# Kernel optimization log

Measured on AMD Instinct MI355X. Metric: run time of the kernel, lower is better.

Reference implementation:

```python
import jax, jax.numpy as jnp
import numpy as np

DIM = 1536
NH = 12
HD = 128
EPS = 1e-6


def _rope(x, freqs, f, h, w, start):
    # x: [B,S,N,D] with S == f*h*w; freqs: [1024, D//2, 2] (real, imag) unit rotations
    B, S, N, D = x.shape
    c = D // 2
    c0 = c - 2 * (c // 3)
    c1 = c // 3
    ff = jnp.broadcast_to(freqs[start:start + f, :c0][:, None, None], (f, h, w, c0, 2))
    fh = jnp.broadcast_to(freqs[:h, c0:c0 + c1][None, :, None], (f, h, w, c1, 2))
    fw = jnp.broadcast_to(freqs[:w, c0 + c1:c][None, None, :], (f, h, w, c1, 2))
    fr = jnp.concatenate([ff, fh, fw], axis=3).reshape(S, 1, c, 2)  # [S,1,c,2]
    xr, xi = x[..., 0::2], x[..., 1::2]          # interleaved real/imag pairs
    cr, ci = fr[None, ..., 0], fr[None, ..., 1]  # [1,S,1,c]
    yr = xr * cr - xi * ci
    yi = xr * ci + xi * cr
    return jnp.stack([yr, yi], axis=-1).reshape(B, S, N, D)


def _rms(x, g):
    return x * jax.lax.rsqrt(jnp.mean(x * x, axis=-1, keepdims=True) + EPS) * g


def setup_inputs():
    key = jax.random.key(0)
    ks = jax.random.split(key, 16)
    S = 3 * 30 * 52  # chunk_size = 3 frames * 1560 tokens/frame
    x = jax.random.normal(ks[0], (1, S, DIM), jnp.float32)
    fr = jax.random.normal(ks[1], (1024, HD // 2, 2), jnp.float32)
    fr = fr / jnp.sqrt(jnp.sum(fr * fr, axis=-1, keepdims=True) + 1e-12)  # unit-modulus rotations
    g_kmean = jax.random.uniform(ks[2], (1, NH, HD), jnp.float32)  # mean of relu(k): nonnegative
    g_kv = jax.random.normal(ks[3], (1, NH, HD, HD), jnp.float32) * 0.05
    p = lambda i, shp: jax.random.normal(ks[i], shp, jnp.float32) * 0.02
    return dict(
        x=x, freqs=fr, g_kmean=g_kmean, g_kv=g_kv,
        Wq=p(4, (DIM, DIM)), bq=p(5, (DIM,)),
        Wk=p(6, (DIM, DIM)), bk=p(7, (DIM,)),
        Wv=p(8, (DIM, DIM)), bv=p(9, (DIM,)),
        Wo=p(10, (DIM, DIM)), bo=p(11, (DIM,)),
        gq=jnp.ones((DIM,), jnp.float32), gk=jnp.ones((DIM,), jnp.float32),
        Wlin=p(12, (HD, HD)), blin=p(13, (HD,)),
        f_frames=3, h_grid=30, w_grid=52,
    )


def reference(x, freqs, g_kmean, g_kv, Wq, bq, Wk, bk, Wv, bv, Wo, bo, gq, gk, Wlin, blin, f_frames, h_grid, w_grid):
    B, S, _ = x.shape
    q = _rms(x @ Wq.T + bq, gq).reshape(B, S, NH, HD)
    k = _rms(x @ Wk.T + bk, gk).reshape(B, S, NH, HD)
    v = (x @ Wv.T + bv).reshape(B, S, NH, HD)
    rq = _rope(q, freqs, f_frames, h_grid, w_grid, 0)
    rk = _rope(k, freqs, f_frames, h_grid, w_grid, 0)
    # local window attention: at step 0 (current_start=0, empty cache, sink_size=0)
    # the working kv window is exactly the roped current chunk
    scores = jnp.einsum('bsnd,btnd->bnst', rq, rk) * (HD ** -0.5)
    x_local = jnp.einsum('bnst,btnd->bsnd', jax.nn.softmax(scores, axis=-1), v)
    # global linear-attention branch (kernel_func = relu feature map on q, roped q against kv state)
    qf = jax.nn.relu(q)
    z = 1.0 / (jnp.einsum('bsnd,bnd->bsn', qf, g_kmean) + 1e-6)
    xg = jnp.einsum('bsnd,bndm->bsnm', rq, g_kv) * z[..., None]
    xg = xg @ Wlin.T + blin
    out = (x_local + xg).reshape(B, S, DIM) @ Wo.T + bo
    return out
```

## Files before the change

### kernel.cpp

```cpp
#include <hip/hip_runtime.h>

typedef short s16x8 __attribute__((ext_vector_type(8)));
typedef float f32x4 __attribute__((ext_vector_type(4)));
typedef unsigned short u16x4 __attribute__((ext_vector_type(4)));

#define QSCALE (0.08838834764831845f * 1.4426950408889634f)

__device__ __forceinline__ unsigned short f2bf(float f) {
  unsigned int u = __float_as_uint(f);
  u += 0x7fffu + ((u >> 16) & 1u);
  return (unsigned short)(u >> 16);
}
__device__ __forceinline__ float bf2f(unsigned short h) {
  return __uint_as_float((unsigned int)h << 16);
}
__device__ __forceinline__ float fast_exp2(float x) {
  float r;
  asm("v_exp_f32 %0, %1" : "=v"(r) : "v"(x));
  return r;
}

__device__ __forceinline__ void gload16(const void* gp, void* lp) {
  __builtin_amdgcn_global_load_lds(
      (const __attribute__((address_space(1))) void*)gp,
      (__attribute__((address_space(3))) void*)lp,
      16, 0, 0);
}

__global__ void cast_f32_bf16_x4(const float* __restrict__ in,
                                 unsigned short* __restrict__ out, int n4) {
  int i = blockIdx.x * 256 + threadIdx.x;
  if (i >= n4) return;
  f32x4 v = *((const f32x4*)in + i);
  u16x4 o;
  o[0] = f2bf(v[0]); o[1] = f2bf(v[1]); o[2] = f2bf(v[2]); o[3] = f2bf(v[3]);
  *((u16x4*)out + i) = o;
}

__global__ void g2fill_kernel(const float* __restrict__ g_kv,
                              const float* __restrict__ Wlin,
                              unsigned short* __restrict__ G2) {
  int h = blockIdx.x, m = blockIdx.y, d = threadIdx.x;
  const float* gk = g_kv + ((size_t)h * 128 + d) * 128;
  const float* wl = Wlin + (size_t)m * 128;
  float s = 0.f;
  for (int j = 0; j < 128; ++j) s += gk[j] * wl[j];
  G2[((size_t)h * 128 + m) * 1536 + h * 128 + d] = f2bf(s * (1.0f / QSCALE));
}

template <int MODE>
__global__ __launch_bounds__(256) void gemm_bt(
    const unsigned short* __restrict__ A, const unsigned short* __restrict__ B,
    const float* __restrict__ bias, void* __restrict__ Cout,
    int M, int N, int K,
    const float* __restrict__ xloc, const float* __restrict__ zbuf) {
  __shared__ __align__(16) unsigned short Asm_[128 * 64];
  __shared__ __align__(16) unsigned short Bsm_[128 * 64];
  const int tid = threadIdx.x;
  const int wid = tid >> 6, lane = tid & 63;
  const int mt = blockIdx.x, nt = blockIdx.y;
  const int wr = wid >> 1, wc = wid & 1;
  f32x4 acc[4][4] = {};

  const int st_srccol = ((((lane & 7) << 4) ^ ((lane >> 3) << 4)) >> 1);
  const int st_rowoff = (lane >> 3);

  for (int k0 = 0; k0 < K; k0 += 64) {
    __syncthreads();
#pragma unroll
    for (int r = 0; r < 4; ++r) {
      int c = wid * 4 + r;
      int lrow = c * 8 + st_rowoff;
      int arow = mt * 128 + lrow; if (arow > M - 1) arow = M - 1;
      gload16(A + (size_t)arow * K + k0 + st_srccol,
              (char*)Asm_ + c * 1024 + lane * 16);
      int brow = nt * 128 + lrow;
      gload16(B + (size_t)brow * K + k0 + st_srccol,
              (char*)Bsm_ + c * 1024 + lane * 16);
    }
    __syncthreads();
#pragma unroll
    for (int kk = 0; kk < 2; ++kk) {
      int cb = (kk * 64 + ((lane >> 4) << 4)) ^ ((lane & 7) << 4);
      s16x8 af[4], bfr[4];
#pragma unroll
      for (int m = 0; m < 4; ++m)
        af[m] = *(const s16x8*)((const char*)Asm_ + (wr * 64 + m * 16 + (lane & 15)) * 128 + cb);
#pragma unroll
      for (int n = 0; n < 4; ++n)
        bfr[n] = *(const s16x8*)((const char*)Bsm_ + (wc * 64 + n * 16 + (lane & 15)) * 128 + cb);
#pragma unroll
      for (int m = 0; m < 4; ++m)
#pragma unroll
        for (int n = 0; n < 4; ++n)
          acc[m][n] = __builtin_amdgcn_mfma_f32_16x16x32_bf16(af[m], bfr[n], acc[m][n], 0, 0, 0);
    }
  }
  const int rb = mt * 128 + wr * 64, cbse = nt * 128 + wc * 64;
#pragma unroll
  for (int m = 0; m < 4; ++m) {
#pragma unroll
    for (int n = 0; n < 4; ++n) {
#pragma unroll
      for (int rg = 0; rg < 4; ++rg) {
        int rr = rb + m * 16 + ((lane >> 4) << 2) + rg;
        int cc = cbse + n * 16 + (lane & 15);
        if (rr < M) {
          float v = acc[m][n][rg];
          if (MODE == 0) {
            v += bias[cc];
            ((unsigned short*)Cout)[(size_t)rr * N + cc] = f2bf(v);
          } else if (MODE == 1) {
            v += bias[cc];
            ((float*)Cout)[(size_t)rr * N + cc] = v;
          } else {
            v = v * zbuf[(size_t)rr * 12 + (cc >> 7)] + xloc[(size_t)rr * N + cc] + bias[cc & 127];
            ((unsigned short*)Cout)[(size_t)rr * N + cc] = f2bf(v);
          }
        }
      }
    }
  }
}

__global__ __launch_bounds__(256) void rms_rope_kernel(
    const unsigned short* __restrict__ pre, const float* __restrict__ freqs,
    const float* __restrict__ g, const float* __restrict__ g_kmean,
    unsigned short* __restrict__ outr, float* __restrict__ zout,
    int S, int ld, float oscale,
    const int* __restrict__ hgp, const int* __restrict__ wgp) {
  const int s = blockIdx.x;
  const int tid = threadIdx.x;
  const int lane = tid & 63, wid = tid >> 6;
  const unsigned short* row = pre + (size_t)s * ld;
  unsigned int pv0, pv1, pv2;
  float ssq = 0.f;
  {
    pv0 = *(const unsigned int*)(row + 2 * (tid));
    pv1 = *(const unsigned int*)(row + 2 * (tid + 256));
    pv2 = *(const unsigned int*)(row + 2 * (tid + 512));
    float a0 = bf2f((unsigned short)(pv0 & 0xffffu)), b0 = bf2f((unsigned short)(pv0 >> 16));
    float a1 = bf2f((unsigned short)(pv1 & 0xffffu)), b1 = bf2f((unsigned short)(pv1 >> 16));
    float a2 = bf2f((unsigned short)(pv2 & 0xffffu)), b2 = bf2f((unsigned short)(pv2 >> 16));
    ssq = a0 * a0 + b0 * b0 + a1 * a1 + b1 * b1 + a2 * a2 + b2 * b2;
  }
#pragma unroll
  for (int m = 1; m < 64; m <<= 1) ssq += __shfl_xor(ssq, m, 64);
  __shared__ float wpart[4];
  if (lane == 0) wpart[wid] = ssq;
  __syncthreads();
  float tot = wpart[0] + wpart[1] + wpart[2] + wpart[3];
  float rms = rsqrtf(tot * (1.0f / 1536.0f) + 1e-6f);
  const int Wg = *wgp;
  const int HWg = (*hgp) * Wg;
  int fi = s / HWg; int rem = s - fi * HWg;
  int hi = rem / Wg; int wi = rem - hi * Wg;
  unsigned int pvs[3] = {pv0, pv1, pv2};
#pragma unroll
  for (int rd = 0; rd < 3; ++rd) {
    int p = tid + rd * 256;
    int c = p & 63;
    int fidx = (c < 22) ? fi : ((c < 43) ? hi : wi);
    float cr = freqs[fidx * 128 + 2 * c];
    float ci = freqs[fidx * 128 + 2 * c + 1];
    float xr = bf2f((unsigned short)(pvs[rd] & 0xffffu)) * rms * g[2 * p];
    float xi = bf2f((unsigned short)(pvs[rd] >> 16)) * rms * g[2 * p + 1];
    float yr = (xr * cr - xi * ci) * oscale;
    float yi = (xr * ci + xi * cr) * oscale;
    unsigned int ow = (unsigned int)f2bf(yr) | ((unsigned int)f2bf(yi) << 16);
    *(unsigned int*)(outr + (size_t)s * 1536 + 2 * p) = ow;
    if (zout != nullptr) {
      int head = p >> 6;
      float part = fmaxf(xr, 0.f) * g_kmean[head * 128 + 2 * c] +
                   fmaxf(xi, 0.f) * g_kmean[head * 128 + 2 * c + 1];
#pragma unroll
      for (int m = 1; m < 64; m <<= 1) part += __shfl_xor(part, m, 64);
      if (lane == 0) zout[(size_t)s * 12 + head] = 1.0f / (part + 1e-6f);
    }
  }
}

__global__ __launch_bounds__(256) void vtrans_kernel(const unsigned short* __restrict__ vpre,
                                                     unsigned short* __restrict__ vt, int S, int ld) {
  __shared__ unsigned short tile[64][66];
  int t0 = blockIdx.x * 64, c0 = blockIdx.y * 64;
  int tid = threadIdx.x;
#pragma unroll
  for (int rep = 0; rep < 16; ++rep) {
    int lin = rep * 256 + tid;
    int i = lin >> 6, j = lin & 63;
    int t = t0 + i; if (t > S - 1) t = S - 1;
    tile[i][j] = vpre[(size_t)t * ld + c0 + j];
  }
  __syncthreads();
#pragma unroll
  for (int rep = 0; rep < 16; ++rep) {
    int lin = rep * 256 + tid;
    int j = lin >> 6, i = lin & 63;
    int t = t0 + i;
    if (t < S) vt[(size_t)(c0 + j) * S + t] = tile[i][j];
  }
}

__global__ __launch_bounds__(256) void attn_kernel(
    const unsigned short* __restrict__ rq, const unsigned short* __restrict__ rk,
    const unsigned short* __restrict__ vt, float* __restrict__ xloc, int S) {
  __shared__ __align__(16) unsigned short Ks[2][64 * 128];
  __shared__ __align__(16) unsigned short Vs[2][64 * 128];
  __shared__ __align__(16) unsigned short Ps[4][32 * 64];
  const int tid = threadIdx.x, wid = tid >> 6, lane = tid & 63;
  const int g = lane >> 4, c = lane & 15;
  const int h = blockIdx.y;
  const int q0 = blockIdx.x * 128 + wid * 32;

  s16x8 qf[2][4];
#pragma unroll
  for (int qh = 0; qh < 2; ++qh) {
    int qrow = q0 + qh * 16 + c; if (qrow > S - 1) qrow = S - 1;
    const unsigned short* qp = rq + (size_t)qrow * 1536 + h * 128 + g * 8;
#pragma unroll
    for (int kk = 0; kk < 4; ++kk) qf[qh][kk] = *(const s16x8*)(qp + kk * 32);
  }
  f32x4 o[2][8] = {};
  float lsum[2] = {0.f, 0.f};
  unsigned short* psw = Ps[wid];

  {
#pragma unroll
    for (int r = 0; r < 4; ++r) {
      int ch = wid * 4 + r;
      int lrow = ch * 4 + (lane >> 4);
      int cb = ((lane & 15) << 4) ^ ((lrow & 7) << 4);
      int trow = lrow; if (trow > S - 1) trow = S - 1;
      gload16(rk + (size_t)trow * 1536 + h * 128 + (cb >> 1),
              (char*)Ks[0] + ch * 1024 + lane * 16);
      int drow = ch * 8 + (lane >> 3);
      int cb2 = ((lane & 7) << 4) ^ ((drow & 7) << 4);
      int tok = (cb2 >> 1); if (tok + 8 > S) tok = S - 8;
      gload16(vt + (size_t)(h * 128 + drow) * S + tok,
              (char*)Vs[0] + ch * 1024 + lane * 16);
    }
  }
  __syncthreads();
  int cur = 0;
  for (int t0 = 0; t0 < S; t0 += 64) {
    if (t0 + 64 < S) {
      int nt0 = t0 + 64;
#pragma unroll
      for (int r = 0; r < 4; ++r) {
        int ch = wid * 4 + r;
        int lrow = ch * 4 + (lane >> 4);
        int cb = ((lane & 15) << 4) ^ ((lrow & 7) << 4);
        int trow = nt0 + lrow; if (trow > S - 1) trow = S - 1;
        gload16(rk + (size_t)trow * 1536 + h * 128 + (cb >> 1),
                (char*)Ks[cur ^ 1] + ch * 1024 + lane * 16);
        int drow = ch * 8 + (lane >> 3);
        int cb2 = ((lane & 7) << 4) ^ ((drow & 7) << 4);
        int tok = nt0 + (cb2 >> 1); if (tok + 8 > S) tok = S - 8;
        gload16(vt + (size_t)(h * 128 + drow) * S + tok,
                (char*)Vs[cur ^ 1] + ch * 1024 + lane * 16);
      }
    }
    f32x4 sc[2][4] = {};
    __builtin_amdgcn_s_setprio(1);
#pragma unroll
    for (int ct = 0; ct < 4; ++ct) {
#pragma unroll
      for (int kk = 0; kk < 4; ++kk) {
        s16x8 kfr = *(const s16x8*)((const char*)Ks[cur] + (ct * 16 + c) * 256 +
                                    ((kk * 64 + (g << 4)) ^ ((c & 7) << 4)));
        sc[0][ct] = __builtin_amdgcn_mfma_f32_16x16x32_bf16(kfr, qf[0][kk], sc[0][ct], 0, 0, 0);
        sc[1][ct] = __builtin_amdgcn_mfma_f32_16x16x32_bf16(kfr, qf[1][kk], sc[1][ct], 0, 0, 0);
      }
    }
    __builtin_amdgcn_s_setprio(0);
    const bool full = (t0 + 64 <= S);
#pragma unroll
    for (int qh = 0; qh < 2; ++qh) {
      float rs0 = 0.f, rs1 = 0.f, rs2 = 0.f, rs3 = 0.f;
      char* prow = (char*)psw + (qh * 16 + c) * 128;
#pragma unroll
      for (int ct = 0; ct < 4; ++ct) {
#pragma unroll
        for (int hh = 0; hh < 2; ++hh) {
          float p0, p1;
          if (full) {
            p0 = fast_exp2(sc[qh][ct][2 * hh]);
            p1 = fast_exp2(sc[qh][ct][2 * hh + 1]);
          } else {
            int T = t0 + ct * 16 + 4 * g + 2 * hh;
            p0 = (T < S) ? fast_exp2(sc[qh][ct][2 * hh]) : 0.f;
            p1 = (T + 1 < S) ? fast_exp2(sc[qh][ct][2 * hh + 1]) : 0.f;
          }
          unsigned int u0 = __float_as_uint(p0) & 0xffff0000u;
          unsigned int u1 = __float_as_uint(p1) & 0xffff0000u;
          if (hh == 0) { rs0 += __uint_as_float(u0); rs1 += __uint_as_float(u1); }
          else         { rs2 += __uint_as_float(u0); rs3 += __uint_as_float(u1); }
          unsigned int w = (u0 >> 16) | u1;
          *(unsigned int*)(prow + ((ct * 32 + 8 * g + 4 * hh) ^ ((c & 7) << 4))) = w;
        }
      }
      lsum[qh] += (rs0 + rs1) + (rs2 + rs3);
    }
    __builtin_amdgcn_s_setprio(1);
#pragma unroll
    for (int kt = 0; kt < 2; ++kt) {
      const int pb = (kt * 64 + (g << 4)) ^ ((c & 7) << 4);
      s16x8 pa0 = *(const s16x8*)((const char*)psw + c * 128 + pb);
      s16x8 pa1 = *(const s16x8*)((const char*)psw + (16 + c) * 128 + pb);
#pragma unroll
      for (int nf = 0; nf < 8; ++nf) {
        s16x8 vfr = *(const s16x8*)((const char*)Vs[cur] + (nf * 16 + c) * 128 + pb);
        o[0][nf] = __builtin_amdgcn_mfma_f32_16x16x32_bf16(pa0, vfr, o[0][nf], 0, 0, 0);
        o[1][nf] = __builtin_amdgcn_mfma_f32_16x16x32_bf16(pa1, vfr, o[1][nf], 0, 0, 0);
      }
    }
    __builtin_amdgcn_s_setprio(0);
    __syncthreads();
    cur ^= 1;
  }
#pragma unroll
  for (int qh = 0; qh < 2; ++qh) {
    float l = lsum[qh];
    l += __shfl_xor(l, 16, 64);
    l += __shfl_xor(l, 32, 64);
    float invl = 1.0f / l;
    f32x4 iv;
#pragma unroll
    for (int rg = 0; rg < 4; ++rg) iv[rg] = __shfl(invl, (g << 2) + rg, 64);
#pragma unroll
    for (int nf = 0; nf < 8; ++nf) {
#pragma unroll
      for (int rg = 0; rg < 4; ++rg) {
        int qrow = q0 + qh * 16 + 4 * g + rg;
        if (qrow < S)
          xloc[(size_t)qrow * 1536 + h * 128 + nf * 16 + c] = o[qh][nf][rg] * iv[rg];
      }
    }
  }
}

extern "C" void kernel_launch(void* const* d_in, const int* in_sizes, int n_in,
                              void* d_out, int out_size, void* d_ws, size_t ws_size,
                              hipStream_t stream) {
  const float* x = (const float*)d_in[0];
  const float* freqs = (const float*)d_in[1];
  const float* g_kmean = (const float*)d_in[2];
  const float* g_kv = (const float*)d_in[3];
  const float* Wq = (const float*)d_in[4];  const float* bq = (const float*)d_in[5];
  const float* Wk = (const float*)d_in[6];  const float* bk = (const float*)d_in[7];
  const float* Wv = (const float*)d_in[8];  const float* bv = (const float*)d_in[9];
  const float* Wo = (const float*)d_in[10]; const float* bo = (const float*)d_in[11];
  const float* gq = (const float*)d_in[12]; const float* gk = (const float*)d_in[13];
  const float* Wlin = (const float*)d_in[14]; const float* blin = (const float*)d_in[15];
  const int* hgp = (const int*)d_in[17];
  const int* wgp = (const int*)d_in[18];

  const int S = in_sizes[0] / 1536;

  char* ws = (char*)d_ws;
  const size_t SZ = (size_t)S * 1536 * 2;
  const size_t WSZ = (size_t)1536 * 1536 * 2;
  const size_t QKVSZ = (size_t)S * 4608 * 2;
  size_t o_xbf = 0;
  size_t o_wqkv = o_xbf + SZ;
  size_t o_wo = o_wqkv + 3 * WSZ;
  size_t o_g2 = o_wo + WSZ;
  size_t o_qkv = o_g2 + WSZ;
  size_t o_rk = o_qkv + QKVSZ;
  size_t o_vt = o_rk + SZ;
  size_t o_z = o_vt + SZ;
  size_t o_bqkv = o_z + (size_t)S * 12 * 4;
  size_t need = o_bqkv + 4608 * 4;
  if (ws_size < need) return;

  unsigned short* xbf = (unsigned short*)(ws + o_xbf);
  unsigned short* wqkv = (unsigned short*)(ws + o_wqkv);
  unsigned short* wob = (unsigned short*)(ws + o_wo);
  unsigned short* g2b = (unsigned short*)(ws + o_g2);
  unsigned short* qkv = (unsigned short*)(ws + o_qkv);
  unsigned short* rkb = (unsigned short*)(ws + o_rk);
  unsigned short* vtb = (unsigned short*)(ws + o_vt);
  float* zbuf = (float*)(ws + o_z);
  float* bqkv = (float*)(ws + o_bqkv);
  unsigned short* rqb = xbf;
  float* xloc = (float*)(ws + o_qkv);
  unsigned short* ybf = (unsigned short*)(ws + o_qkv + 2 * SZ);

  {
    int n4 = (S * 1536) / 4;
    cast_f32_bf16_x4<<<(n4 + 255) / 256, 256, 0, stream>>>(x, xbf, n4);
    int w4 = (1536 * 1536) / 4;
    int wg = (w4 + 255) / 256;
    cast_f32_bf16_x4<<<wg, 256, 0, stream>>>(Wq, wqkv, w4);
    cast_f32_bf16_x4<<<wg, 256, 0, stream>>>(Wk, wqkv + (size_t)1536 * 1536, w4);
    cast_f32_bf16_x4<<<wg, 256, 0, stream>>>(Wv, wqkv + (size_t)2 * 1536 * 1536, w4);
    cast_f32_bf16_x4<<<wg, 256, 0, stream>>>(Wo, wob, w4);
  }
  hipMemcpyAsync(bqkv, bq, 1536 * 4, hipMemcpyDeviceToDevice, stream);
  hipMemcpyAsync(bqkv + 1536, bk, 1536 * 4, hipMemcpyDeviceToDevice, stream);
  hipMemcpyAsync(bqkv + 3072, bv, 1536 * 4, hipMemcpyDeviceToDevice, stream);

  hipMemsetAsync(g2b, 0, WSZ, stream);
  g2fill_kernel<<<dim3(12, 128), 128, 0, stream>>>(g_kv, Wlin, g2b);

  {
    dim3 ggrid((S + 127) / 128, 36);
    gemm_bt<0><<<ggrid, 256, 0, stream>>>(xbf, wqkv, bqkv, qkv, S, 4608, 1536, nullptr, nullptr);
  }

  rms_rope_kernel<<<S, 256, 0, stream>>>(qkv, freqs, gq, g_kmean, rqb, zbuf, S, 4608, QSCALE, hgp, wgp);
  rms_rope_kernel<<<S, 256, 0, stream>>>(qkv + 1536, freqs, gk, nullptr, rkb, nullptr, S, 4608, 1.0f, hgp, wgp);

  vtrans_kernel<<<dim3((S + 63) / 64, 24), 256, 0, stream>>>(qkv + 3072, vtb, S, 4608);

  attn_kernel<<<dim3((S + 127) / 128, 12), 256, 0, stream>>>(rqb, rkb, vtb, xloc, S);

  {
    dim3 ggrid((S + 127) / 128, 12);
    gemm_bt<2><<<ggrid, 256, 0, stream>>>(rqb, g2b, blin, ybf, S, 1536, 1536, xloc, zbuf);
    gemm_bt<1><<<ggrid, 256, 0, stream>>>(ybf, wob, bo, (float*)d_out, S, 1536, 1536, nullptr, nullptr);
  }
}
```

Baseline: 480.2 us.

## Split attention KV range across two blocks and merge partial sums in GEMM epilogue

Launches attention with a second grid dimension that splits the key/value sequence into two halves. Each half writes unnormalized fp32 output and row sums to separate buffers. The MODE 2 GEMM epilogue adds the two partials and divides by the combined sum. The KV tile shrinks from 64 to 32 tokens to cut LDS use and allow higher occupancy. The aim is to fill the GPU better, at the cost of extra fp32 partial-output traffic and more loop iterations.

```diff
diff --git a/kernel.cpp b/kernel.cpp
--- a/kernel.cpp
+++ b/kernel.cpp
@@ -53,7 +53,8 @@
     const unsigned short* __restrict__ A, const unsigned short* __restrict__ B,
     const float* __restrict__ bias, void* __restrict__ Cout,
     int M, int N, int K,
-    const float* __restrict__ xloc, const float* __restrict__ zbuf) {
+    const float* __restrict__ o0buf, const float* __restrict__ zbuf,
+    const float* __restrict__ o1buf, const float* __restrict__ lbuf) {
   __shared__ __align__(16) unsigned short Asm_[128 * 64];
   __shared__ __align__(16) unsigned short Bsm_[128 * 64];
   const int tid = threadIdx.x;
@@ -114,7 +115,10 @@
             v += bias[cc];
             ((float*)Cout)[(size_t)rr * N + cc] = v;
           } else {
-            v = v * zbuf[(size_t)rr * 12 + (cc >> 7)] + xloc[(size_t)rr * N + cc] + bias[cc & 127];
+            int hd = cc >> 7;
+            float lsum = lbuf[(size_t)rr * 12 + hd] + lbuf[(size_t)(M + rr) * 12 + hd];
+            float osum = o0buf[(size_t)rr * N + cc] + o1buf[(size_t)rr * N + cc];
+            v = v * zbuf[(size_t)rr * 12 + hd] + osum * (1.0f / lsum) + bias[cc & 127];
             ((unsigned short*)Cout)[(size_t)rr * N + cc] = f2bf(v);
           }
         }
@@ -202,16 +206,23 @@
   }
 }
 
-__global__ __launch_bounds__(256) void attn_kernel(
+__global__ __launch_bounds__(256, 4) void attn_kernel(
     const unsigned short* __restrict__ rq, const unsigned short* __restrict__ rk,
-    const unsigned short* __restrict__ vt, float* __restrict__ xloc, int S) {
-  __shared__ __align__(16) unsigned short Ks[2][64 * 128];
-  __shared__ __align__(16) unsigned short Vs[2][64 * 128];
-  __shared__ __align__(16) unsigned short Ps[4][32 * 64];
+    const unsigned short* __restrict__ vt, float* __restrict__ o0buf,
+    float* __restrict__ o1buf, float* __restrict__ lbuf, int S) {
+  __shared__ __align__(16) unsigned short Ks[2][32 * 128];
+  __shared__ __align__(16) unsigned short Vs[2][128 * 32];
+  __shared__ __align__(16) unsigned short Ps[4][32 * 32];
   const int tid = threadIdx.x, wid = tid >> 6, lane = tid & 63;
   const int g = lane >> 4, c = lane & 15;
   const int h = blockIdx.y;
   const int q0 = blockIdx.x * 128 + wid * 32;
+  const int z = blockIdx.z;
+  const int SP = ((S / 2) + 31) & ~31;
+  const int tbeg = z ? SP : 0;
+  const int tend = z ? S : SP;
+  float* obufz = z ? o1buf : o0buf;
+  float* lbufz = lbuf + (size_t)z * S * 12;
 
   s16x8 qf[2][4];
 #pragma unroll
@@ -225,46 +236,49 @@
   float lsum[2] = {0.f, 0.f};
   unsigned short* psw = Ps[wid];
 
+  const int k_lrow_base = (lane >> 4);
+  const int k_cbyte = ((lane & 15) << 4);
+  const int v_row_off = (lane >> 2);
+  const int v_tok_off = (lane & 3) * 8;
+
   {
 #pragma unroll
-    for (int r = 0; r < 4; ++r) {
-      int ch = wid * 4 + r;
-      int lrow = ch * 4 + (lane >> 4);
-      int cb = ((lane & 15) << 4) ^ ((lrow & 7) << 4);
-      int trow = lrow; if (trow > S - 1) trow = S - 1;
+    for (int r = 0; r < 2; ++r) {
+      int ch = wid * 2 + r;
+      int lrow = ch * 4 + k_lrow_base;
+      int cb = k_cbyte ^ ((lrow & 7) << 4);
+      int trow = tbeg + lrow; if (trow > S - 1) trow = S - 1;
       gload16(rk + (size_t)trow * 1536 + h * 128 + (cb >> 1),
               (char*)Ks[0] + ch * 1024 + lane * 16);
-      int drow = ch * 8 + (lane >> 3);
-      int cb2 = ((lane & 7) << 4) ^ ((drow & 7) << 4);
-      int tok = (cb2 >> 1); if (tok + 8 > S) tok = S - 8;
-      gload16(vt + (size_t)(h * 128 + drow) * S + tok,
+      int vrow = ch * 16 + v_row_off;
+      int tok = tbeg + v_tok_off; if (tok > S - 8) tok = S - 8;
+      gload16(vt + (size_t)(h * 128 + vrow) * S + tok,
               (char*)Vs[0] + ch * 1024 + lane * 16);
     }
   }
   __syncthreads();
   int cur = 0;
-  for (int t0 = 0; t0 < S; t0 += 64) {
-    if (t0 + 64 < S) {
-      int nt0 = t0 + 64;
-#pragma unroll
-      for (int r = 0; r < 4; ++r) {
-        int ch = wid * 4 + r;
-        int lrow = ch * 4 + (lane >> 4);
-        int cb = ((lane & 15) << 4) ^ ((lrow & 7) << 4);
+  for (int t0 = tbeg; t0 < tend; t0 += 32) {
+    if (t0 + 32 < tend) {
+      int nt0 = t0 + 32;
+#pragma unroll
+      for (int r = 0; r < 2; ++r) {
+        int ch = wid * 2 + r;
+        int lrow = ch * 4 + k_lrow_base;
+        int cb = k_cbyte ^ ((lrow & 7) << 4);
         int trow = nt0 + lrow; if (trow > S - 1) trow = S - 1;
         gload16(rk + (size_t)trow * 1536 + h * 128 + (cb >> 1),
                 (char*)Ks[cur ^ 1] + ch * 1024 + lane * 16);
-        int drow = ch * 8 + (lane >> 3);
-        int cb2 = ((lane & 7) << 4) ^ ((drow & 7) << 4);
-        int tok = nt0 + (cb2 >> 1); if (tok + 8 > S) tok = S - 8;
-        gload16(vt + (size_t)(h * 128 + drow) * S + tok,
+        int vrow = ch * 16 + v_row_off;
+        int tok = nt0 + v_tok_off; if (tok > S - 8) tok = S - 8;
+        gload16(vt + (size_t)(h * 128 + vrow) * S + tok,
                 (char*)Vs[cur ^ 1] + ch * 1024 + lane * 16);
       }
     }
-    f32x4 sc[2][4] = {};
+    f32x4 sc[2][2] = {};
     __builtin_amdgcn_s_setprio(1);
 #pragma unroll
-    for (int ct = 0; ct < 4; ++ct) {
+    for (int ct = 0; ct < 2; ++ct) {
 #pragma unroll
       for (int kk = 0; kk < 4; ++kk) {
         s16x8 kfr = *(const s16x8*)((const char*)Ks[cur] + (ct * 16 + c) * 256 +
@@ -274,43 +288,46 @@
       }
     }
     __builtin_amdgcn_s_setprio(0);
-    const bool full = (t0 + 64 <= S);
+    const bool full = (t0 + 32 <= tend);
+    const int psw_swz = (c & 3) << 4;
 #pragma unroll
     for (int qh = 0; qh < 2; ++qh) {
-      float rs0 = 0.f, rs1 = 0.f, rs2 = 0.f, rs3 = 0.f;
-      char* prow = (char*)psw + (qh * 16 + c) * 128;
-#pragma unroll
-      for (int ct = 0; ct < 4; ++ct) {
-#pragma unroll
-        for (int hh = 0; hh < 2; ++hh) {
-          float p0, p1;
-          if (full) {
-            p0 = fast_exp2(sc[qh][ct][2 * hh]);
-            p1 = fast_exp2(sc[qh][ct][2 * hh + 1]);
-          } else {
-            int T = t0 + ct * 16 + 4 * g + 2 * hh;
-            p0 = (T < S) ? fast_exp2(sc[qh][ct][2 * hh]) : 0.f;
-            p1 = (T + 1 < S) ? fast_exp2(sc[qh][ct][2 * hh + 1]) : 0.f;
-          }
-          unsigned int u0 = __float_as_uint(p0) & 0xffff0000u;
-          unsigned int u1 = __float_as_uint(p1) & 0xffff0000u;
-          if (hh == 0) { rs0 += __uint_as_float(u0); rs1 += __uint_as_float(u1); }
-          else         { rs2 += __uint_as_float(u0); rs3 += __uint_as_float(u1); }
-          unsigned int w = (u0 >> 16) | u1;
-          *(unsigned int*)(prow + ((ct * 32 + 8 * g + 4 * hh) ^ ((c & 7) << 4))) = w;
+      float rs = 0.f;
+      char* prow = (char*)psw + (qh * 16 + c) * 64;
+#pragma unroll
+      for (int ct = 0; ct < 2; ++ct) {
+        float p0, p1, p2, p3;
+        if (full) {
+          p0 = fast_exp2(sc[qh][ct][0]); p1 = fast_exp2(sc[qh][ct][1]);
+          p2 = fast_exp2(sc[qh][ct][2]); p3 = fast_exp2(sc[qh][ct][3]);
+        } else {
+          int T = t0 + ct * 16 + 4 * g;
+          p0 = (T < tend) ? fast_exp2(sc[qh][ct][0]) : 0.f;
+          p1 = (T + 1 < tend) ? fast_exp2(sc[qh][ct][1]) : 0.f;
+          p2 = (T + 2 < tend) ? fast_exp2(sc[qh][ct][2]) : 0.f;
+          p3 = (T + 3 < tend) ? fast_exp2(sc[qh][ct][3]) : 0.f;
         }
-      }
-      lsum[qh] += (rs0 + rs1) + (rs2 + rs3);
+        unsigned int u0 = __float_as_uint(p0) & 0xffff0000u;
+        unsigned int u1 = __float_as_uint(p1) & 0xffff0000u;
+        unsigned int u2 = __float_as_uint(p2) & 0xffff0000u;
+        unsigned int u3 = __float_as_uint(p3) & 0xffff0000u;
+        rs += (__uint_as_float(u0) + __uint_as_float(u1)) +
+              (__uint_as_float(u2) + __uint_as_float(u3));
+        uint2 w;
+        w.x = (u0 >> 16) | u1;
+        w.y = (u2 >> 16) | u3;
+        *(uint2*)(prow + ((ct * 32 + 8 * g) ^ psw_swz)) = w;
+      }
+      lsum[qh] += rs;
     }
     __builtin_amdgcn_s_setprio(1);
-#pragma unroll
-    for (int kt = 0; kt < 2; ++kt) {
-      const int pb = (kt * 64 + (g << 4)) ^ ((c & 7) << 4);
-      s16x8 pa0 = *(const s16x8*)((const char*)psw + c * 128 + pb);
-      s16x8 pa1 = *(const s16x8*)((const char*)psw + (16 + c) * 128 + pb);
+    {
+      const int pbp = 16 * (g ^ (c & 3));
+      s16x8 pa0 = *(const s16x8*)((const char*)psw + c * 64 + pbp);
+      s16x8 pa1 = *(const s16x8*)((const char*)psw + (16 + c) * 64 + pbp);
 #pragma unroll
       for (int nf = 0; nf < 8; ++nf) {
-        s16x8 vfr = *(const s16x8*)((const char*)Vs[cur] + (nf * 16 + c) * 128 + pb);
+        s16x8 vfr = *(const s16x8*)((const char*)Vs[cur] + (nf * 16 + c) * 64 + 16 * g);
         o[0][nf] = __builtin_amdgcn_mfma_f32_16x16x32_bf16(pa0, vfr, o[0][nf], 0, 0, 0);
         o[1][nf] = __builtin_amdgcn_mfma_f32_16x16x32_bf16(pa1, vfr, o[1][nf], 0, 0, 0);
       }
@@ -324,17 +341,17 @@
     float l = lsum[qh];
     l += __shfl_xor(l, 16, 64);
     l += __shfl_xor(l, 32, 64);
-    float invl = 1.0f / l;
-    f32x4 iv;
-#pragma unroll
-    for (int rg = 0; rg < 4; ++rg) iv[rg] = __shfl(invl, (g << 2) + rg, 64);
+    if (g == 0) {
+      int qrow = q0 + qh * 16 + c;
+      if (qrow < S) lbufz[(size_t)qrow * 12 + h] = l;
+    }
 #pragma unroll
     for (int nf = 0; nf < 8; ++nf) {
 #pragma unroll
       for (int rg = 0; rg < 4; ++rg) {
         int qrow = q0 + qh * 16 + 4 * g + rg;
         if (qrow < S)
-          xloc[(size_t)qrow * 1536 + h * 128 + nf * 16 + c] = o[qh][nf][rg] * iv[rg];
+          obufz[(size_t)qrow * 1536 + h * 128 + nf * 16 + c] = o[qh][nf][rg];
       }
     }
   }
@@ -371,7 +388,9 @@
   size_t o_vt = o_rk + SZ;
   size_t o_z = o_vt + SZ;
   size_t o_bqkv = o_z + (size_t)S * 12 * 4;
-  size_t need = o_bqkv + 4608 * 4;
+  size_t o_o1 = o_bqkv + 4608 * 4;
+  size_t o_l = o_o1 + 2 * SZ;
+  size_t need = o_l + (size_t)2 * S * 12 * 4;
   if (ws_size < need) return;
 
   unsigned short* xbf = (unsigned short*)(ws + o_xbf);
@@ -384,7 +403,9 @@
   float* zbuf = (float*)(ws + o_z);
   float* bqkv = (float*)(ws + o_bqkv);
   unsigned short* rqb = xbf;
-  float* xloc = (float*)(ws + o_qkv);
+  float* o0buf = (float*)(ws + o_qkv);
+  float* o1buf = (float*)(ws + o_o1);
+  float* lbuf = (float*)(ws + o_l);
   unsigned short* ybf = (unsigned short*)(ws + o_qkv + 2 * SZ);
 
   {
@@ -406,7 +427,8 @@
 
   {
     dim3 ggrid((S + 127) / 128, 36);
-    gemm_bt<0><<<ggrid, 256, 0, stream>>>(xbf, wqkv, bqkv, qkv, S, 4608, 1536, nullptr, nullptr);
+    gemm_bt<0><<<ggrid, 256, 0, stream>>>(xbf, wqkv, bqkv, qkv, S, 4608, 1536,
+                                          nullptr, nullptr, nullptr, nullptr);
   }
 
   rms_rope_kernel<<<S, 256, 0, stream>>>(qkv, freqs, gq, g_kmean, rqb, zbuf, S, 4608, QSCALE, hgp, wgp);
@@ -414,11 +436,14 @@
 
   vtrans_kernel<<<dim3((S + 63) / 64, 24), 256, 0, stream>>>(qkv + 3072, vtb, S, 4608);
 
-  attn_kernel<<<dim3((S + 127) / 128, 12), 256, 0, stream>>>(rqb, rkb, vtb, xloc, S);
+  attn_kernel<<<dim3((S + 127) / 128, 12, 2), 256, 0, stream>>>(rqb, rkb, vtb,
+                                                                o0buf, o1buf, lbuf, S);
 
   {
     dim3 ggrid((S + 127) / 128, 12);
-    gemm_bt<2><<<ggrid, 256, 0, stream>>>(rqb, g2b, blin, ybf, S, 1536, 1536, xloc, zbuf);
-    gemm_bt<1><<<ggrid, 256, 0, stream>>>(ybf, wob, bo, (float*)d_out, S, 1536, 1536, nullptr, nullptr);
-  }
-}
+    gemm_bt<2><<<ggrid, 256, 0, stream>>>(rqb, g2b, blin, ybf, S, 1536, 1536,
+                                          o0buf, zbuf, o1buf, lbuf);
+    gemm_bt<1><<<ggrid, 256, 0, stream>>>(ybf, wob, bo, (float*)d_out, S, 1536, 1536,
+                                          nullptr, nullptr, nullptr, nullptr);
+  }
+}
```

New measurement: 560.3 us. 1.17x slower.
